# Kernel tuning notes

Hardware: AMD Instinct MI355X
Metric: run time of the kernel (lower is better)

## Reference

```python
import jax, jax.numpy as jnp
import numpy as np

EPS = 1e-5
P = 3  # p_size
BW = 1.0  # bandwidth


def _instance_norm(x):
    # calc_mean_std: per (B,C) mean/std over spatial dims, unbiased var (torch default)
    b, c, h, w = x.shape
    flat = x.reshape(b, c, h * w)
    mean = flat.mean(-1)[:, :, None, None]
    std = jnp.sqrt(flat.var(-1, ddof=1) + EPS)[:, :, None, None]
    return (x - mean) / std


def _conv1x1(x, w, bias):
    # x: (B,C,H,W), w: (O,C), bias: (O,)
    return jnp.einsum('oc,bchw->bohw', w, x) + bias[None, :, None, None]


def _patches_scaled(x, scale):
    # ReflectionPad2d(1) + Unfold(3) -> (B, HW, C*9), torch layout (c slow, k fast),
    # with ContextAtten scale applied over the 9 kernel positions.
    b, c, h, w = x.shape
    pad = jnp.pad(x, ((0, 0), (0, 0), (1, 1), (1, 1)), mode='reflect')
    # (B,C,H,W,9)
    p9 = jnp.stack([pad[:, :, di:di + h, dj:dj + w]
                    for di in range(P) for dj in range(P)], axis=-1)
    p9 = p9 * scale  # broadcast over last (kernel) axis
    # -> (B,H,W,C,9) -> (B, HW, C*9)
    return p9.transpose(0, 2, 3, 1, 4).reshape(b, h * w, c * P * P)


def setup_inputs() -> dict:
    key = jax.random.key(0)
    ks = jax.random.split(key, 12)
    B, C, H, W = 2, 512, 64, 64
    IC = 256
    f32 = jnp.float32
    inp = {
        'content': jax.random.normal(ks[0], (B, C, H, W), f32),
        'style': jax.random.normal(ks[1], (B, C, H, W), f32),
        'fusion_style': jax.random.normal(ks[2], (B, C, H, W), f32),
        'theta_w': jax.random.normal(ks[3], (IC, C), f32) * np.sqrt(2.0 / C),
        'theta_b': jnp.zeros((IC,), f32),
        'phi_w': jax.random.normal(ks[4], (IC, C), f32) * np.sqrt(2.0 / C),
        'phi_b': jnp.zeros((IC,), f32),
        'g_w': jax.random.normal(ks[5], (IC, C), f32) * np.sqrt(2.0 / C),
        'g_b': jnp.zeros((IC,), f32),
        'W_w': jax.random.normal(ks[6], (C, IC), f32) * np.sqrt(2.0 / IC),
        'W_b': jnp.zeros((C,), f32),
        'scale': jnp.ones((P * P,), f32),
    }
    return inp


def reference(content, style, fusion_style, theta_w, theta_b, phi_w, phi_b,
              g_w, g_b, W_w, W_b, scale):
    B, C, H, W = content.shape
    IC = theta_w.shape[0]
    HW = H * W

    # g on fusion_style -> (B, HW, IC)
    g_s = _conv1x1(fusion_style, g_w, g_b).reshape(B, IC, HW).transpose(0, 2, 1)

    # instance-normalize content/style (normal=True path)
    xn = _instance_norm(content)
    sn = _instance_norm(style)

    theta_x = _conv1x1(xn, theta_w, theta_b)
    phi_s = _conv1x1(sn, phi_w, phi_b)

    theta_p = _patches_scaled(theta_x, scale)  # (B, HW, IC*9)
    phi_p = _patches_scaled(phi_s, scale)      # (B, HW, IC*9)

    f = jnp.einsum('blk,bmk->blm', theta_p, phi_p) * BW  # (B, HW, HW)
    f_div_C = jax.nn.softmax(f, axis=-1)

    y = jnp.einsum('blm,bmo->blo', f_div_C, g_s)  # (B, HW, IC)
    y = y.transpose(0, 2, 1).reshape(B, IC, H, W)
    W_y = _conv1x1(y, W_w, W_b)  # (B, C, H, W)
    # isTraining=True path: conf_map = 0
    return W_y
```

## Files before the change

### kernel.cpp

```cpp
#include <hip/hip_runtime.h>
#include <stdint.h>

typedef __attribute__((ext_vector_type(8))) __bf16 bf16x8;
typedef __attribute__((ext_vector_type(4))) float f32x4;
typedef __attribute__((ext_vector_type(4))) unsigned int uint4v;

__device__ __forceinline__ float bf2f(unsigned short u){
  unsigned int x = ((unsigned int)u) << 16;
  return __builtin_bit_cast(float, x);
}
__device__ __forceinline__ unsigned short f2bf(float f){
  unsigned int x = __builtin_bit_cast(unsigned int, f);
  x += 0x7FFFu + ((x >> 16) & 1u);
  return (unsigned short)(x >> 16);
}

#define OUT_F32 0
#define OUT_BF16 1
#define OUT_SPLIT3 2
#define OUT_FLAG 3
#define OUT_PART 4
#define OUT_PARTH 5
#define BIAS_NONE 0
#define BIAS_ROW 1
#define BIAS_COL 2

template<int OM, int BM>
__global__ __launch_bounds__(256)
void gemm_bt(const unsigned short* __restrict__ A, int lda,
             const unsigned short* __restrict__ Bt, int ldb,
             int kchunk, void* __restrict__ Out, int ldo,
             const float* __restrict__ bias,
             int dupOff, int loOff,
             const unsigned int* __restrict__ flagPtr, size_t outOff,
             size_t zStride)
{
  __shared__ uint4v AsmBuf[1024];
  __shared__ uint4v BsmBuf[1024];
  char* Asm = (char*)AsmBuf;
  char* Bsm = (char*)BsmBuf;

  const unsigned int fl = (OM == OUT_FLAG) ? flagPtr[0] : 0u;

  const int tid  = threadIdx.x;
  const int lane = tid & 63;
  const int wave = tid >> 6;
  const int wy = wave >> 1, wx = wave & 1;
  const int lm = lane & 15, quad = lane >> 4;
  const int tileM = blockIdx.y * 128;
  const int tileN = blockIdx.x * 128;
  const int z = blockIdx.z;

  A  += (size_t)z * kchunk;
  Bt += (size_t)z * kchunk;

  const int sr0 = tid >> 2, sc0 = tid & 3;
  const int sr1 = sr0 + 64;
  const size_t gA0 = (size_t)(tileM + sr0)*lda + ((sc0 ^ ((sr0 >> 1) & 3)) << 3);
  const size_t gA1 = (size_t)(tileM + sr1)*lda + ((sc0 ^ ((sr1 >> 1) & 3)) << 3);
  const size_t gB0 = (size_t)(tileN + sr0)*ldb + ((sc0 ^ ((sr0 >> 1) & 3)) << 3);
  const size_t gB1 = (size_t)(tileN + sr1)*ldb + ((sc0 ^ ((sr1 >> 1) & 3)) << 3);
  const int lOff0 = sr0*64 + sc0*16;
  const int lOff1 = sr1*64 + sc0*16;

  int aOff[4], bOff[4];
#pragma unroll
  for (int t = 0; t < 4; ++t){
    int ra = wy*64 + t*16 + lm;
    aOff[t] = ra*64 + ((quad ^ ((ra >> 1) & 3)) << 4);
    int rb = wx*64 + t*16 + lm;
    bOff[t] = rb*64 + ((quad ^ ((rb >> 1) & 3)) << 4);
  }

  f32x4 acc[4][4] = {};

  const int ksteps = kchunk >> 5;
  uint4v a0v = *(const uint4v*)(A + gA0);
  uint4v a1v = *(const uint4v*)(A + gA1);
  uint4v b0v = *(const uint4v*)(Bt + gB0);
  uint4v b1v = *(const uint4v*)(Bt + gB1);

  for (int kt = 0; kt < ksteps; ++kt){
    char* As = Asm + (kt & 1)*8192;
    char* Bs = Bsm + (kt & 1)*8192;
    *(uint4v*)(As + lOff0) = a0v;
    *(uint4v*)(As + lOff1) = a1v;
    *(uint4v*)(Bs + lOff0) = b0v;
    *(uint4v*)(Bs + lOff1) = b1v;
    __syncthreads();
    if (kt + 1 < ksteps){
      const unsigned short* Ak = A + (kt + 1)*32;
      const unsigned short* Bk = Bt + (kt + 1)*32;
      a0v = *(const uint4v*)(Ak + gA0);
      a1v = *(const uint4v*)(Ak + gA1);
      b0v = *(const uint4v*)(Bk + gB0);
      b1v = *(const uint4v*)(Bk + gB1);
    }
    bf16x8 af[4], bfr[4];
#pragma unroll
    for (int t = 0; t < 4; ++t){
      af[t]  = __builtin_bit_cast(bf16x8, *(const uint4v*)(As + aOff[t]));
      bfr[t] = __builtin_bit_cast(bf16x8, *(const uint4v*)(Bs + bOff[t]));
    }
#pragma unroll
    for (int tm = 0; tm < 4; ++tm)
#pragma unroll
      for (int tn = 0; tn < 4; ++tn)
        acc[tm][tn] = __builtin_amdgcn_mfma_f32_16x16x32_bf16(af[tm], bfr[tn], acc[tm][tn], 0, 0, 0);
  }

#pragma unroll
  for (int tm = 0; tm < 4; ++tm){
    const int rowb = tileM + wy*64 + tm*16 + quad*4;
#pragma unroll
    for (int tn = 0; tn < 4; ++tn){
      const int col = tileN + wx*64 + tn*16 + lm;
      float bcv = 0.f;
      if (BM == BIAS_COL) bcv = bias[col];
#pragma unroll
      for (int r = 0; r < 4; ++r){
        float v = acc[tm][tn][r];
        const int row = rowb + r;
        if (BM == BIAS_ROW) v += bias[row];
        if (BM == BIAS_COL) v += bcv;
        const size_t idx = (size_t)row*ldo + col;
        if (OM == OUT_F32){
          ((float*)Out)[idx] = v;
        } else if (OM == OUT_BF16){
          ((unsigned short*)Out)[idx] = f2bf(v);
        } else if (OM == OUT_SPLIT3){
          unsigned short hi = f2bf(v);
          unsigned short lo = f2bf(v - bf2f(hi));
          unsigned short* O = (unsigned short*)Out;
          O[idx] = hi; O[idx + dupOff] = hi; O[idx + loOff] = lo;
        } else if (OM == OUT_PART){
          ((float*)Out)[(size_t)z*zStride + idx] = v;
        } else if (OM == OUT_PARTH){
          ((unsigned short*)Out)[(size_t)z*zStride + idx] = f2bf(v);
        } else {
          if (fl) ((float*)Out)[outOff + idx] = v;
          else    ((unsigned short*)Out)[outOff + idx] = f2bf(v);
        }
      }
    }
  }
}

__global__ __launch_bounds__(256)
void gemm_big(const unsigned short* __restrict__ A, int lda,
              const unsigned short* __restrict__ Bt, int ldb,
              int K, float* __restrict__ Out, int ldo)
{
  __shared__ uint4v AsmBuf[2048];
  __shared__ uint4v BsmBuf[1024];
  char* Asm = (char*)AsmBuf;
  char* Bsm = (char*)BsmBuf;

  const int tid  = threadIdx.x;
  const int lane = tid & 63;
  const int wave = tid >> 6;
  const int wy = wave >> 1, wx = wave & 1;
  const int lm = lane & 15, quad = lane >> 4;
  const int tileM = blockIdx.y * 256;
  const int tileN = blockIdx.x * 128;

  const int sr = tid >> 2, sc = tid & 3;
  size_t gA[4]; int lA[4];
  size_t gB[2]; int lB[2];
#pragma unroll
  for (int i = 0; i < 4; ++i){
    const int r = sr + 64*i;
    gA[i] = (size_t)(tileM + r)*lda + ((sc ^ ((r >> 1) & 3)) << 3);
    lA[i] = r*64 + sc*16;
  }
#pragma unroll
  for (int i = 0; i < 2; ++i){
    const int r = sr + 64*i;
    gB[i] = (size_t)(tileN + r)*ldb + ((sc ^ ((r >> 1) & 3)) << 3);
    lB[i] = r*64 + sc*16;
  }

  int aOff[8], bOff[4];
#pragma unroll
  for (int t = 0; t < 8; ++t){
    const int ra = wy*128 + t*16 + lm;
    aOff[t] = ra*64 + ((quad ^ ((ra >> 1) & 3)) << 4);
  }
#pragma unroll
  for (int t = 0; t < 4; ++t){
    const int rb = wx*64 + t*16 + lm;
    bOff[t] = rb*64 + ((quad ^ ((rb >> 1) & 3)) << 4);
  }

  f32x4 acc[8][4] = {};

  const int ksteps = K >> 5;
  uint4v av[4], bv[2];
#pragma unroll
  for (int i = 0; i < 4; ++i) av[i] = *(const uint4v*)(A + gA[i]);
#pragma unroll
  for (int i = 0; i < 2; ++i) bv[i] = *(const uint4v*)(Bt + gB[i]);

  for (int kt = 0; kt < ksteps; ++kt){
    char* As = Asm + (kt & 1)*16384;
    char* Bs = Bsm + (kt & 1)*8192;
#pragma unroll
    for (int i = 0; i < 4; ++i) *(uint4v*)(As + lA[i]) = av[i];
#pragma unroll
    for (int i = 0; i < 2; ++i) *(uint4v*)(Bs + lB[i]) = bv[i];
    __syncthreads();
    if (kt + 1 < ksteps){
      const unsigned short* Ak = A + (kt + 1)*32;
      const unsigned short* Bk = Bt + (kt + 1)*32;
#pragma unroll
      for (int i = 0; i < 4; ++i) av[i] = *(const uint4v*)(Ak + gA[i]);
#pragma unroll
      for (int i = 0; i < 2; ++i) bv[i] = *(const uint4v*)(Bk + gB[i]);
    }
    bf16x8 af[8], bfr[4];
#pragma unroll
    for (int t = 0; t < 8; ++t)
      af[t] = __builtin_bit_cast(bf16x8, *(const uint4v*)(As + aOff[t]));
#pragma unroll
    for (int t = 0; t < 4; ++t)
      bfr[t] = __builtin_bit_cast(bf16x8, *(const uint4v*)(Bs + bOff[t]));
#pragma unroll
    for (int tm = 0; tm < 8; ++tm)
#pragma unroll
      for (int tn = 0; tn < 4; ++tn)
        acc[tm][tn] = __builtin_amdgcn_mfma_f32_16x16x32_bf16(af[tm], bfr[tn], acc[tm][tn], 0, 0, 0);
  }

#pragma unroll
  for (int tm = 0; tm < 8; ++tm){
    const int rowb = tileM + wy*128 + tm*16 + quad*4;
#pragma unroll
    for (int tn = 0; tn < 4; ++tn){
      const int col = tileN + wx*64 + tn*16 + lm;
#pragma unroll
      for (int r = 0; r < 4; ++r)
        Out[(size_t)(rowb + r)*ldo + col] = acc[tm][tn][r];
    }
  }
}

template<int S, int OM, int BM, int CSH, bool HALFP>
__global__ __launch_bounds__(256)
void reduce_part(const void* __restrict__ part, size_t zStride,
                 const float* __restrict__ bias,
                 void* __restrict__ Out, int ldo,
                 int dupOff, int loOff,
                 const unsigned int* __restrict__ flagPtr, size_t outOff)
{
  const size_t i = (size_t)blockIdx.x*256 + threadIdx.x;
  const int row = (int)(i >> CSH);
  const int col = (int)(i & ((1u << CSH) - 1u));
  float v = 0.f;
#pragma unroll
  for (int s = 0; s < S; ++s){
    if (HALFP) v += bf2f(((const unsigned short*)part)[(size_t)s*zStride + i]);
    else       v += ((const float*)part)[(size_t)s*zStride + i];
  }
  if (BM == BIAS_ROW) v += bias[row];
  if (BM == BIAS_COL) v += bias[col];
  const size_t o = (size_t)row*ldo + col;
  if (OM == OUT_SPLIT3){
    unsigned short hi = f2bf(v);
    unsigned short lo = f2bf(v - bf2f(hi));
    unsigned short* O = (unsigned short*)Out;
    O[o] = hi; O[o + dupOff] = hi; O[o + loOff] = lo;
  } else if (OM == OUT_BF16){
    ((unsigned short*)Out)[o] = f2bf(v);
  } else {
    if (flagPtr[0]) ((float*)Out)[outOff + o] = v;
    else            ((unsigned short*)Out)[outOff + o] = f2bf(v);
  }
}

__global__ __launch_bounds__(256)
void detect_prep(const void* __restrict__ content,
                 const void* tb, const void* pb, const void* gb, const void* wb,
                 const void* sc,
                 unsigned int* __restrict__ flag, float* __restrict__ scale_c,
                 float* tb_c, float* pb_c, float* gb_c, float* wb_c)
{
  __shared__ int cnt;
  __shared__ unsigned int flg;
  const int tid = threadIdx.x;
  if (tid == 0) cnt = 0;
  __syncthreads();
  unsigned int w = ((const unsigned int*)content)[tid];
  int e = (w >> 23) & 0xFF;
  if (e >= 0x70 && e <= 0x8F) atomicAdd(&cnt, 1);
  __syncthreads();
  if (tid == 0){ flg = (cnt >= 128) ? 1u : 0u; flag[0] = flg; }
  __syncthreads();
  const unsigned int f = flg;
  auto rd = [&](const void* p, int i)->float{
    return f ? ((const float*)p)[i] : bf2f(((const unsigned short*)p)[i]);
  };
  if (tid < 9) scale_c[tid] = rd(sc, tid);
  tb_c[tid] = rd(tb, tid);
  pb_c[tid] = rd(pb, tid);
  gb_c[tid] = rd(gb, tid);
  wb_c[tid] = rd(wb, tid);
  wb_c[tid + 256] = rd(wb, tid + 256);
}

__global__ __launch_bounds__(256)
void conv_weights(const void* tw, const void* pw, const void* gw, const void* www,
                  const unsigned int* __restrict__ flagPtr,
                  unsigned short* __restrict__ wdup,
                  unsigned short* __restrict__ gwc,
                  unsigned short* __restrict__ wwc)
{
  const unsigned int fl = flagPtr[0];
  const int sec = blockIdx.y;
  const int idx = blockIdx.x*256 + threadIdx.x;
  auto rd = [&](const void* p, int i)->float{
    return fl ? ((const float*)p)[i] : bf2f(((const unsigned short*)p)[i]);
  };
  if (sec < 2){
    const void* w = sec ? pw : tw;
    const int o = idx >> 9, c = idx & 511;
    float v = rd(w, o*512 + c);
    unsigned short hi = f2bf(v);
    unsigned short lo = f2bf(v - bf2f(hi));
    unsigned short* base = wdup + (size_t)sec*256*1536 + o*1536;
    base[c] = hi; base[512 + c] = lo; base[1024 + c] = hi;
  } else if (sec == 2){
    const int o = idx >> 9, c = idx & 511;
    gwc[o*512 + c] = f2bf(rd(gw, o*512 + c));
  } else {
    const int o = idx >> 8, c = idx & 255;
    wwc[o*256 + c] = f2bf(rd(www, o*256 + c));
  }
}

__global__ __launch_bounds__(256)
void stats_kernel(const void* __restrict__ X, const unsigned int* __restrict__ flagPtr,
                  float* __restrict__ stats)
{
  const unsigned int fl = flagPtr[0];
  const int bc = blockIdx.x;
  const int tid = threadIdx.x;
  float s = 0.f, q = 0.f;
  if (fl){
    const f32x4* row = (const f32x4*)((const float*)X + (size_t)bc*4096);
#pragma unroll
    for (int i = 0; i < 4; ++i){
      f32x4 v = row[tid + i*256];
#pragma unroll
      for (int j = 0; j < 4; ++j){ s += v[j]; q += v[j]*v[j]; }
    }
  } else {
    const uint4v* row = (const uint4v*)((const unsigned short*)X + (size_t)bc*4096);
#pragma unroll
    for (int i = 0; i < 2; ++i){
      uint4v u = row[tid + i*256];
#pragma unroll
      for (int j = 0; j < 4; ++j){
        float a = bf2f((unsigned short)(u[j] & 0xffffu));
        float b = bf2f((unsigned short)(u[j] >> 16));
        s += a + b; q += a*a + b*b;
      }
    }
  }
#pragma unroll
  for (int off = 32; off > 0; off >>= 1){
    s += __shfl_down(s, off);
    q += __shfl_down(q, off);
  }
  __shared__ float rs[4], rq[4];
  if ((tid & 63) == 0){ rs[tid >> 6] = s; rq[tid >> 6] = q; }
  __syncthreads();
  if (tid == 0){
    s = rs[0] + rs[1] + rs[2] + rs[3];
    q = rq[0] + rq[1] + rq[2] + rq[3];
    float mean = s * (1.0f/4096.0f);
    float var  = (q - 4096.0f*mean*mean) * (1.0f/4095.0f);
    stats[bc*2 + 0] = mean;
    stats[bc*2 + 1] = 1.0f / sqrtf(var + 1e-5f);
  }
}

template<bool SPLIT>
__global__ __launch_bounds__(256)
void norm_transpose(const void* __restrict__ X, const float* __restrict__ stats,
                    unsigned short* __restrict__ Out,
                    const unsigned int* __restrict__ flagPtr)
{
  __shared__ float tile[64][65];
  const unsigned int fl = flagPtr[0];
  const int b  = blockIdx.z;
  const int l0 = blockIdx.x * 64;
  const int c0 = blockIdx.y * 64;
  const int tid = threadIdx.x;
  const int tx = tid & 63, ty = tid >> 6;

#pragma unroll
  for (int p = 0; p < 16; ++p){
    const int cc = ty + p*4;
    const size_t src = ((size_t)b*512 + c0 + cc)*4096 + l0 + tx;
    tile[cc][tx] = fl ? ((const float*)X)[src]
                      : bf2f(((const unsigned short*)X)[src]);
  }
  __syncthreads();
  float mean = 0.f, inv = 1.f;
  if (SPLIT){
    mean = stats[(b*512 + c0 + tx)*2 + 0];
    inv  = stats[(b*512 + c0 + tx)*2 + 1];
  }
#pragma unroll
  for (int p = 0; p < 16; ++p){
    const int lj = ty + p*4;
    const size_t rowOut = (size_t)b*4096 + l0 + lj;
    if (SPLIT){
      const float v = (tile[tx][lj] - mean) * inv;
      const size_t o = rowOut*1536 + c0 + tx;
      const unsigned short hi = f2bf(v);
      Out[o] = hi;
      Out[o + 512] = hi;
      Out[o + 1024] = f2bf(v - bf2f(hi));
    } else {
      const size_t o = rowOut*512 + c0 + tx;
      Out[o] = f2bf(tile[tx][lj]);
    }
  }
}

__global__ __launch_bounds__(256)
void softmax_rows(const float* __restrict__ G, const float* __restrict__ scale_c,
                  unsigned short* __restrict__ P)
{
  const int l = blockIdx.x;
  const int yy = l >> 6, xx = l & 63;
  const int tid = threadIdx.x;

  float s2[9];
  const float* rowp[9];
#pragma unroll
  for (int di = 0; di < 3; ++di){
    int ry = yy + di - 1; ry = ry < 0 ? 1 : (ry > 63 ? 62 : ry);
#pragma unroll
    for (int dj = 0; dj < 3; ++dj){
      int rx = xx + dj - 1; rx = rx < 0 ? 1 : (rx > 63 ? 62 : rx);
      const int k = di*3 + dj;
      const float s = scale_c[k];
      s2[k] = s*s;
      rowp[k] = G + (size_t)(ry*64 + rx)*4096;
    }
  }

  float fv[16];
  float mx = -3.0e38f;
#pragma unroll
  for (int i = 0; i < 16; ++i){
    const int m = tid + i*256;
    const int my = m >> 6, mxo = m & 63;
    int cy[3], cx[3];
#pragma unroll
    for (int d = 0; d < 3; ++d){
      int t0 = my + d - 1;  cy[d] = (t0 < 0 ? 1 : (t0 > 63 ? 62 : t0))*64;
      int t1 = mxo + d - 1; cx[d] = (t1 < 0 ? 1 : (t1 > 63 ? 62 : t1));
    }
    float v = 0.f;
#pragma unroll
    for (int di = 0; di < 3; ++di)
#pragma unroll
      for (int dj = 0; dj < 3; ++dj)
        v = fmaf(s2[di*3+dj], rowp[di*3+dj][cy[di] + cx[dj]], v);
    fv[i] = v;
    mx = fmaxf(mx, v);
  }

  __shared__ float redA[4], redB[4];
#pragma unroll
  for (int off = 32; off > 0; off >>= 1) mx = fmaxf(mx, __shfl_down(mx, off));
  if ((tid & 63) == 0) redA[tid >> 6] = mx;
  __syncthreads();
  mx = fmaxf(fmaxf(redA[0], redA[1]), fmaxf(redA[2], redA[3]));

  float sum = 0.f;
#pragma unroll
  for (int i = 0; i < 16; ++i){ fv[i] = __expf(fv[i] - mx); sum += fv[i]; }
#pragma unroll
  for (int off = 32; off > 0; off >>= 1) sum += __shfl_down(sum, off);
  if ((tid & 63) == 0) redB[tid >> 6] = sum;
  __syncthreads();
  sum = redB[0] + redB[1] + redB[2] + redB[3];
  const float inv = 1.0f / sum;

  unsigned short* Prow = P + (size_t)l*4096;
#pragma unroll
  for (int i = 0; i < 16; ++i) Prow[tid + i*256] = f2bf(fv[i]*inv);
}

extern "C" void kernel_launch(void* const* d_in, const int* in_sizes, int n_in,
                              void* d_out, int out_size, void* d_ws, size_t ws_size,
                              hipStream_t stream)
{
  const void* content = d_in[0];
  const void* style   = d_in[1];
  const void* fusion  = d_in[2];
  const void* theta_w = d_in[3];
  const void* theta_b = d_in[4];
  const void* phi_w   = d_in[5];
  const void* phi_b   = d_in[6];
  const void* g_w     = d_in[7];
  const void* g_b     = d_in[8];
  const void* W_w     = d_in[9];
  const void* W_b     = d_in[10];
  const void* scale   = d_in[11];

  char* ws = (char*)d_ws;
  size_t off = 0;
  auto take = [&](size_t bytes)->char*{
    char* p = ws + off; off += (bytes + 255) & ~(size_t)255; return p;
  };

  unsigned int* flag  = (unsigned int*)take(256);
  float* scale_c      = (float*)take(256);
  float* tb_c         = (float*)take(1024);
  float* pb_c         = (float*)take(1024);
  float* gb_c         = (float*)take(1024);
  float* wb_c         = (float*)take(2048);
  float* statsC       = (float*)take(1024ull*2*4);
  float* statsS       = (float*)take(1024ull*2*4);
  unsigned short* wdup = (unsigned short*)take(2ull*256*1536*2);
  unsigned short* gwc  = (unsigned short*)take(256ull*512*2);
  unsigned short* wwc  = (unsigned short*)take(512ull*256*2);
  unsigned short* th   = (unsigned short*)take(8192ull*768*2);
  unsigned short* ph   = (unsigned short*)take(8192ull*768*2);
  unsigned short* gs   = (unsigned short*)take(256ull*8192*2);
  unsigned short* yb   = (unsigned short*)take(2ull*4096*256*2);
  float* G             = (float*)take(4096ull*4096*4);
  char* unionC         = take(2ull*4096*1536*2*2 + 2ull*4096*512*2);
  unsigned short* xn   = (unsigned short*)unionC;
  unsigned short* sn   = (unsigned short*)(unionC + 8192ull*1536*2);
  unsigned short* fst  = (unsigned short*)(unionC + 2ull*8192*1536*2);
  unsigned short* P    = (unsigned short*)unionC;
  float* partF          = G;
  unsigned short* partH = (unsigned short*)G;
  const size_t zTP = 8192ull*256;
  const size_t zG  = 256ull*8192;
  const size_t zY  = 4096ull*256;
  const size_t zW  = 512ull*4096;

  detect_prep<<<1, 256, 0, stream>>>(content, theta_b, phi_b, g_b, W_b, scale,
                                     flag, scale_c, tb_c, pb_c, gb_c, wb_c);
  conv_weights<<<dim3(512,4), 256, 0, stream>>>(theta_w, phi_w, g_w, W_w, flag,
                                                wdup, gwc, wwc);
  stats_kernel<<<1024, 256, 0, stream>>>(content, flag, statsC);
  stats_kernel<<<1024, 256, 0, stream>>>(style,   flag, statsS);
  dim3 ntg(64, 8, 2);
  norm_transpose<true ><<<ntg, 256, 0, stream>>>(content, statsC, xn, flag);
  norm_transpose<true ><<<ntg, 256, 0, stream>>>(style,   statsS, sn, flag);
  norm_transpose<false><<<ntg, 256, 0, stream>>>(fusion,  nullptr, fst, flag);

  gemm_bt<OUT_PART, BIAS_NONE><<<dim3(2,64,4), 256, 0, stream>>>(
      xn, 1536, wdup, 1536, 384, partF, 256, nullptr, 0, 0, nullptr, 0, zTP);
  reduce_part<4, OUT_SPLIT3, BIAS_COL, 8, false><<<8192, 256, 0, stream>>>(
      partF, zTP, tb_c, th, 768, 256, 512, nullptr, 0);
  gemm_bt<OUT_PART, BIAS_NONE><<<dim3(2,64,4), 256, 0, stream>>>(
      sn, 1536, wdup + 256*1536, 1536, 384, partF, 256, nullptr, 0, 0, nullptr, 0, zTP);
  reduce_part<4, OUT_SPLIT3, BIAS_COL, 8, false><<<8192, 256, 0, stream>>>(
      partF, zTP, pb_c, ph, 768, 512, 256, nullptr, 0);
  gemm_bt<OUT_PARTH, BIAS_NONE><<<dim3(64,2,4), 256, 0, stream>>>(
      gwc, 512, fst, 512, 128, partH, 8192, nullptr, 0, 0, nullptr, 0, zG);
  reduce_part<4, OUT_BF16, BIAS_ROW, 13, true><<<8192, 256, 0, stream>>>(
      partH, zG, gb_c, gs, 8192, 0, 0, nullptr, 0);

  for (int b = 0; b < 2; ++b){
    const unsigned short* thb = th + (size_t)b*4096*768;
    const unsigned short* phb = ph + (size_t)b*4096*768;
    gemm_big<<<dim3(32,16), 256, 0, stream>>>(thb, 768, phb, 768, 768, G, 4096);
    softmax_rows<<<4096, 256, 0, stream>>>(G, scale_c, P);
    gemm_bt<OUT_PARTH, BIAS_NONE><<<dim3(2,32,8), 256, 0, stream>>>(
        P, 4096, gs + (size_t)b*4096, 8192, 512, partH, 256, nullptr, 0, 0, nullptr, 0, zY);
    reduce_part<8, OUT_BF16, BIAS_NONE, 8, true><<<4096, 256, 0, stream>>>(
        partH, zY, nullptr, yb + (size_t)b*4096*256, 256, 0, 0, nullptr, 0);
    gemm_bt<OUT_PART, BIAS_NONE><<<dim3(32,4,2), 256, 0, stream>>>(
        wwc, 256, yb + (size_t)b*4096*256, 256, 128, partF, 4096, nullptr, 0, 0, nullptr, 0, zW);
    reduce_part<2, OUT_FLAG, BIAS_ROW, 12, false><<<8192, 256, 0, stream>>>(
        partF, zW, wb_c, d_out, 4096, 0, 0, flag, (size_t)b*512*4096);
  }
}
```

Before: 418.4 us.

## Batch per-batch and per-input launches into single grid-z kernels

Merges the two batch iterations and the paired content/style/fusion launches into single launches by indexing the batch or input through blockIdx.z. The stats, normalize, projection GEMMs, the big similarity GEMM, softmax, the aggregation GEMM and the output GEMM each run once with a doubled grid, and a second 64 MB score buffer is allocated so both batches' scores coexist. Reductions get specialized kernels. This is meant to cut launch count and fill the GPU better on the smaller GEMMs, at the cost of more memory footprint.

```diff
diff --git a/kernel.cpp b/kernel.cpp
--- a/kernel.cpp
+++ b/kernel.cpp
@@ -15,32 +15,21 @@
   return (unsigned short)(x >> 16);
 }
 
-#define OUT_F32 0
-#define OUT_BF16 1
-#define OUT_SPLIT3 2
-#define OUT_FLAG 3
 #define OUT_PART 4
 #define OUT_PARTH 5
-#define BIAS_NONE 0
-#define BIAS_ROW 1
-#define BIAS_COL 2
-
-template<int OM, int BM>
+
+template<int OM>
 __global__ __launch_bounds__(256)
 void gemm_bt(const unsigned short* __restrict__ A, int lda,
              const unsigned short* __restrict__ Bt, int ldb,
              int kchunk, void* __restrict__ Out, int ldo,
-             const float* __restrict__ bias,
-             int dupOff, int loOff,
-             const unsigned int* __restrict__ flagPtr, size_t outOff,
-             size_t zStride)
+             size_t zStride, size_t aBatch, size_t bBatch,
+             int sMask, int sShift)
 {
   __shared__ uint4v AsmBuf[1024];
   __shared__ uint4v BsmBuf[1024];
   char* Asm = (char*)AsmBuf;
   char* Bsm = (char*)BsmBuf;
-
-  const unsigned int fl = (OM == OUT_FLAG) ? flagPtr[0] : 0u;
 
   const int tid  = threadIdx.x;
   const int lane = tid & 63;
@@ -50,9 +39,11 @@
   const int tileM = blockIdx.y * 128;
   const int tileN = blockIdx.x * 128;
   const int z = blockIdx.z;
-
-  A  += (size_t)z * kchunk;
-  Bt += (size_t)z * kchunk;
+  const int slice = z & sMask;
+  const int batch = z >> sShift;
+
+  A  += (size_t)slice*kchunk + (size_t)batch*aBatch;
+  Bt += (size_t)slice*kchunk + (size_t)batch*bBatch;
 
   const int sr0 = tid >> 2, sc0 = tid & 3;
   const int sr1 = sr0 + 64;
@@ -115,32 +106,12 @@
 #pragma unroll
     for (int tn = 0; tn < 4; ++tn){
       const int col = tileN + wx*64 + tn*16 + lm;
-      float bcv = 0.f;
-      if (BM == BIAS_COL) bcv = bias[col];
 #pragma unroll
       for (int r = 0; r < 4; ++r){
-        float v = acc[tm][tn][r];
-        const int row = rowb + r;
-        if (BM == BIAS_ROW) v += bias[row];
-        if (BM == BIAS_COL) v += bcv;
-        const size_t idx = (size_t)row*ldo + col;
-        if (OM == OUT_F32){
-          ((float*)Out)[idx] = v;
-        } else if (OM == OUT_BF16){
-          ((unsigned short*)Out)[idx] = f2bf(v);
-        } else if (OM == OUT_SPLIT3){
-          unsigned short hi = f2bf(v);
-          unsigned short lo = f2bf(v - bf2f(hi));
-          unsigned short* O = (unsigned short*)Out;
-          O[idx] = hi; O[idx + dupOff] = hi; O[idx + loOff] = lo;
-        } else if (OM == OUT_PART){
-          ((float*)Out)[(size_t)z*zStride + idx] = v;
-        } else if (OM == OUT_PARTH){
-          ((unsigned short*)Out)[(size_t)z*zStride + idx] = f2bf(v);
-        } else {
-          if (fl) ((float*)Out)[outOff + idx] = v;
-          else    ((unsigned short*)Out)[outOff + idx] = f2bf(v);
-        }
+        const float v = acc[tm][tn][r];
+        const size_t idx = (size_t)z*zStride + (size_t)(rowb + r)*ldo + col;
+        if (OM == OUT_PART) ((float*)Out)[idx] = v;
+        else                ((unsigned short*)Out)[idx] = f2bf(v);
       }
     }
   }
@@ -149,7 +120,8 @@
 __global__ __launch_bounds__(256)
 void gemm_big(const unsigned short* __restrict__ A, int lda,
               const unsigned short* __restrict__ Bt, int ldb,
-              int K, float* __restrict__ Out, int ldo)
+              int K, float* __restrict__ Out, int ldo,
+              size_t aBatch, size_t bBatch, size_t oBatch)
 {
   __shared__ uint4v AsmBuf[2048];
   __shared__ uint4v BsmBuf[1024];
@@ -163,6 +135,11 @@
   const int lm = lane & 15, quad = lane >> 4;
   const int tileM = blockIdx.y * 256;
   const int tileN = blockIdx.x * 128;
+  const int z = blockIdx.z;
+
+  A  += (size_t)z*aBatch;
+  Bt += (size_t)z*bBatch;
+  Out += (size_t)z*oBatch;
 
   const int sr = tid >> 2, sc = tid & 3;
   size_t gA[4]; int lA[4];
@@ -244,37 +221,66 @@
   }
 }
 
-template<int S, int OM, int BM, int CSH, bool HALFP>
-__global__ __launch_bounds__(256)
-void reduce_part(const void* __restrict__ part, size_t zStride,
-                 const float* __restrict__ bias,
-                 void* __restrict__ Out, int ldo,
-                 int dupOff, int loOff,
-                 const unsigned int* __restrict__ flagPtr, size_t outOff)
+__global__ __launch_bounds__(256)
+void reduce_tp(const float* __restrict__ part,
+               const float* __restrict__ tb, const float* __restrict__ pb,
+               unsigned short* __restrict__ th, unsigned short* __restrict__ ph)
 {
   const size_t i = (size_t)blockIdx.x*256 + threadIdx.x;
-  const int row = (int)(i >> CSH);
-  const int col = (int)(i & ((1u << CSH) - 1u));
+  const int which = (int)(i >> 21);
+  const size_t j = i & 0x1FFFFFu;
+  const int col = (int)(j & 255u);
   float v = 0.f;
 #pragma unroll
-  for (int s = 0; s < S; ++s){
-    if (HALFP) v += bf2f(((const unsigned short*)part)[(size_t)s*zStride + i]);
-    else       v += ((const float*)part)[(size_t)s*zStride + i];
-  }
-  if (BM == BIAS_ROW) v += bias[row];
-  if (BM == BIAS_COL) v += bias[col];
-  const size_t o = (size_t)row*ldo + col;
-  if (OM == OUT_SPLIT3){
-    unsigned short hi = f2bf(v);
-    unsigned short lo = f2bf(v - bf2f(hi));
-    unsigned short* O = (unsigned short*)Out;
-    O[o] = hi; O[o + dupOff] = hi; O[o + loOff] = lo;
-  } else if (OM == OUT_BF16){
-    ((unsigned short*)Out)[o] = f2bf(v);
-  } else {
-    if (flagPtr[0]) ((float*)Out)[outOff + o] = v;
-    else            ((unsigned short*)Out)[outOff + o] = f2bf(v);
-  }
+  for (int s = 0; s < 4; ++s)
+    v += part[(size_t)((which << 2) + s)*2097152 + j];
+  v += (which ? pb : tb)[col];
+  unsigned short hi = f2bf(v);
+  unsigned short lo = f2bf(v - bf2f(hi));
+  const size_t o = (j >> 8)*768 + col;
+  unsigned short* O = which ? ph : th;
+  const int dup = which ? 512 : 256;
+  const int loo = which ? 256 : 512;
+  O[o] = hi; O[o + dup] = hi; O[o + loo] = lo;
+}
+
+__global__ __launch_bounds__(256)
+void reduce_g(const unsigned short* __restrict__ part,
+              const float* __restrict__ gb, unsigned short* __restrict__ gs)
+{
+  const size_t i = (size_t)blockIdx.x*256 + threadIdx.x;
+  float v = 0.f;
+#pragma unroll
+  for (int s = 0; s < 4; ++s) v += bf2f(part[(size_t)s*2097152 + i]);
+  gs[i] = f2bf(v + gb[i >> 13]);
+}
+
+__global__ __launch_bounds__(256)
+void reduce_y(const unsigned short* __restrict__ part,
+              unsigned short* __restrict__ yb)
+{
+  const size_t i = (size_t)blockIdx.x*256 + threadIdx.x;
+  const int b = (int)(i >> 20);
+  const size_t j = i & 0xFFFFFu;
+  float v = 0.f;
+#pragma unroll
+  for (int s = 0; s < 8; ++s)
+    v += bf2f(part[(size_t)((b << 3) + s)*1048576 + j]);
+  yb[i] = f2bf(v);
+}
+
+__global__ __launch_bounds__(256)
+void reduce_w(const float* __restrict__ part, const float* __restrict__ wb,
+              void* __restrict__ Out, const unsigned int* __restrict__ flagPtr)
+{
+  const size_t i = (size_t)blockIdx.x*256 + threadIdx.x;
+  const int b = (int)(i >> 21);
+  const size_t j = i & 0x1FFFFFu;
+  float v = part[(size_t)(b << 1)*2097152 + j]
+          + part[(size_t)((b << 1) | 1)*2097152 + j]
+          + wb[(i >> 12) & 511u];
+  if (flagPtr[0]) ((float*)Out)[i] = v;
+  else            ((unsigned short*)Out)[i] = f2bf(v);
 }
 
 __global__ __launch_bounds__(256)
@@ -338,10 +344,13 @@
 }
 
 __global__ __launch_bounds__(256)
-void stats_kernel(const void* __restrict__ X, const unsigned int* __restrict__ flagPtr,
-                  float* __restrict__ stats)
+void stats_all(const void* __restrict__ content, const void* __restrict__ style,
+               const unsigned int* __restrict__ flagPtr,
+               float* __restrict__ statsC, float* __restrict__ statsS)
 {
   const unsigned int fl = flagPtr[0];
+  const void* X = blockIdx.z ? style : content;
+  float* stats = blockIdx.z ? statsS : statsC;
   const int bc = blockIdx.x;
   const int tid = threadIdx.x;
   float s = 0.f, q = 0.f;
@@ -384,20 +393,25 @@
   }
 }
 
-template<bool SPLIT>
-__global__ __launch_bounds__(256)
-void norm_transpose(const void* __restrict__ X, const float* __restrict__ stats,
-                    unsigned short* __restrict__ Out,
-                    const unsigned int* __restrict__ flagPtr)
+__global__ __launch_bounds__(256)
+void norm_all(const void* __restrict__ content, const void* __restrict__ style,
+              const void* __restrict__ fusion,
+              const float* __restrict__ statsC, const float* __restrict__ statsS,
+              unsigned short* __restrict__ xn, unsigned short* __restrict__ sn,
+              unsigned short* __restrict__ fst,
+              const unsigned int* __restrict__ flagPtr)
 {
   __shared__ float tile[64][65];
   const unsigned int fl = flagPtr[0];
-  const int b  = blockIdx.z;
+  const int z = blockIdx.z;
+  const int which = z >> 1;
+  const int b  = z & 1;
   const int l0 = blockIdx.x * 64;
   const int c0 = blockIdx.y * 64;
   const int tid = threadIdx.x;
   const int tx = tid & 63, ty = tid >> 6;
 
+  const void* X = which == 0 ? content : (which == 1 ? style : fusion);
 #pragma unroll
   for (int p = 0; p < 16; ++p){
     const int cc = ty + p*4;
@@ -406,34 +420,39 @@
                       : bf2f(((const unsigned short*)X)[src]);
   }
   __syncthreads();
-  float mean = 0.f, inv = 1.f;
-  if (SPLIT){
-    mean = stats[(b*512 + c0 + tx)*2 + 0];
-    inv  = stats[(b*512 + c0 + tx)*2 + 1];
-  }
-#pragma unroll
-  for (int p = 0; p < 16; ++p){
-    const int lj = ty + p*4;
-    const size_t rowOut = (size_t)b*4096 + l0 + lj;
-    if (SPLIT){
+  if (which < 2){
+    const float* stats = which ? statsS : statsC;
+    const float mean = stats[(b*512 + c0 + tx)*2 + 0];
+    const float inv  = stats[(b*512 + c0 + tx)*2 + 1];
+    unsigned short* Out = which ? sn : xn;
+#pragma unroll
+    for (int p = 0; p < 16; ++p){
+      const int lj = ty + p*4;
       const float v = (tile[tx][lj] - mean) * inv;
-      const size_t o = rowOut*1536 + c0 + tx;
+      const size_t o = ((size_t)b*4096 + l0 + lj)*1536 + c0 + tx;
       const unsigned short hi = f2bf(v);
       Out[o] = hi;
       Out[o + 512] = hi;
       Out[o + 1024] = f2bf(v - bf2f(hi));
-    } else {
-      const size_t o = rowOut*512 + c0 + tx;
-      Out[o] = f2bf(tile[tx][lj]);
-    }
-  }
-}
-
-__global__ __launch_bounds__(256)
-void softmax_rows(const float* __restrict__ G, const float* __restrict__ scale_c,
-                  unsigned short* __restrict__ P)
-{
-  const int l = blockIdx.x;
+    }
+  } else {
+#pragma unroll
+    for (int p = 0; p < 16; ++p){
+      const int lj = ty + p*4;
+      const size_t o = ((size_t)b*4096 + l0 + lj)*512 + c0 + tx;
+      fst[o] = f2bf(tile[tx][lj]);
+    }
+  }
+}
+
+__global__ __launch_bounds__(256)
+void softmax_rows(const float* __restrict__ Gbase, const float* __restrict__ scale_c,
+                  unsigned short* __restrict__ Pbase)
+{
+  const int bb = blockIdx.x >> 12;
+  const int l  = blockIdx.x & 4095;
+  const float* G = Gbase + (size_t)bb*16777216;
+  unsigned short* P = Pbase + (size_t)bb*16777216;
   const int yy = l >> 6, xx = l & 63;
   const int tid = threadIdx.x;
 
@@ -534,55 +553,49 @@
   unsigned short* ph   = (unsigned short*)take(8192ull*768*2);
   unsigned short* gs   = (unsigned short*)take(256ull*8192*2);
   unsigned short* yb   = (unsigned short*)take(2ull*4096*256*2);
-  float* G             = (float*)take(4096ull*4096*4);
-  char* unionC         = take(2ull*4096*1536*2*2 + 2ull*4096*512*2);
+  float* G0            = (float*)take(4096ull*4096*4);
+  float* G1            = (float*)take(4096ull*4096*4);
+  char* unionC         = take(64ull*1024*1024);
   unsigned short* xn   = (unsigned short*)unionC;
   unsigned short* sn   = (unsigned short*)(unionC + 8192ull*1536*2);
   unsigned short* fst  = (unsigned short*)(unionC + 2ull*8192*1536*2);
   unsigned short* P    = (unsigned short*)unionC;
-  float* partF          = G;
-  unsigned short* partH = (unsigned short*)G;
-  const size_t zTP = 8192ull*256;
-  const size_t zG  = 256ull*8192;
-  const size_t zY  = 4096ull*256;
-  const size_t zW  = 512ull*4096;
+
+  float* partTP          = G0;
+  unsigned short* partG  = (unsigned short*)G1;
+  unsigned short* partY  = (unsigned short*)G0;
+  float* partW           = G1;
 
   detect_prep<<<1, 256, 0, stream>>>(content, theta_b, phi_b, g_b, W_b, scale,
                                      flag, scale_c, tb_c, pb_c, gb_c, wb_c);
   conv_weights<<<dim3(512,4), 256, 0, stream>>>(theta_w, phi_w, g_w, W_w, flag,
                                                 wdup, gwc, wwc);
-  stats_kernel<<<1024, 256, 0, stream>>>(content, flag, statsC);
-  stats_kernel<<<1024, 256, 0, stream>>>(style,   flag, statsS);
-  dim3 ntg(64, 8, 2);
-  norm_transpose<true ><<<ntg, 256, 0, stream>>>(content, statsC, xn, flag);
-  norm_transpose<true ><<<ntg, 256, 0, stream>>>(style,   statsS, sn, flag);
-  norm_transpose<false><<<ntg, 256, 0, stream>>>(fusion,  nullptr, fst, flag);
-
-  gemm_bt<OUT_PART, BIAS_NONE><<<dim3(2,64,4), 256, 0, stream>>>(
-      xn, 1536, wdup, 1536, 384, partF, 256, nullptr, 0, 0, nullptr, 0, zTP);
-  reduce_part<4, OUT_SPLIT3, BIAS_COL, 8, false><<<8192, 256, 0, stream>>>(
-      partF, zTP, tb_c, th, 768, 256, 512, nullptr, 0);
-  gemm_bt<OUT_PART, BIAS_NONE><<<dim3(2,64,4), 256, 0, stream>>>(
-      sn, 1536, wdup + 256*1536, 1536, 384, partF, 256, nullptr, 0, 0, nullptr, 0, zTP);
-  reduce_part<4, OUT_SPLIT3, BIAS_COL, 8, false><<<8192, 256, 0, stream>>>(
-      partF, zTP, pb_c, ph, 768, 512, 256, nullptr, 0);
-  gemm_bt<OUT_PARTH, BIAS_NONE><<<dim3(64,2,4), 256, 0, stream>>>(
-      gwc, 512, fst, 512, 128, partH, 8192, nullptr, 0, 0, nullptr, 0, zG);
-  reduce_part<4, OUT_BF16, BIAS_ROW, 13, true><<<8192, 256, 0, stream>>>(
-      partH, zG, gb_c, gs, 8192, 0, 0, nullptr, 0);
-
-  for (int b = 0; b < 2; ++b){
-    const unsigned short* thb = th + (size_t)b*4096*768;
-    const unsigned short* phb = ph + (size_t)b*4096*768;
-    gemm_big<<<dim3(32,16), 256, 0, stream>>>(thb, 768, phb, 768, 768, G, 4096);
-    softmax_rows<<<4096, 256, 0, stream>>>(G, scale_c, P);
-    gemm_bt<OUT_PARTH, BIAS_NONE><<<dim3(2,32,8), 256, 0, stream>>>(
-        P, 4096, gs + (size_t)b*4096, 8192, 512, partH, 256, nullptr, 0, 0, nullptr, 0, zY);
-    reduce_part<8, OUT_BF16, BIAS_NONE, 8, true><<<4096, 256, 0, stream>>>(
-        partH, zY, nullptr, yb + (size_t)b*4096*256, 256, 0, 0, nullptr, 0);
-    gemm_bt<OUT_PART, BIAS_NONE><<<dim3(32,4,2), 256, 0, stream>>>(
-        wwc, 256, yb + (size_t)b*4096*256, 256, 128, partF, 4096, nullptr, 0, 0, nullptr, 0, zW);
-    reduce_part<2, OUT_FLAG, BIAS_ROW, 12, false><<<8192, 256, 0, stream>>>(
-        partF, zW, wb_c, d_out, 4096, 0, 0, flag, (size_t)b*512*4096);
-  }
-}
+  stats_all<<<dim3(1024,1,2), 256, 0, stream>>>(content, style, flag, statsC, statsS);
+  norm_all<<<dim3(64,8,6), 256, 0, stream>>>(content, style, fusion,
+                                             statsC, statsS, xn, sn, fst, flag);
+
+  gemm_bt<OUT_PART><<<dim3(2,64,8), 256, 0, stream>>>(
+      xn, 1536, wdup, 1536, 384, partTP, 256, 8192ull*256,
+      8192ull*1536, 256ull*1536, 3, 2);
+  reduce_tp<<<16384, 256, 0, stream>>>(partTP, tb_c, pb_c, th, ph);
+
+  gemm_bt<OUT_PARTH><<<dim3(64,2,4), 256, 0, stream>>>(
+      gwc, 512, fst, 512, 128, partG, 8192, 256ull*8192, 0, 0, 3, 2);
+  reduce_g<<<8192, 256, 0, stream>>>(partG, gb_c, gs);
+
+  gemm_big<<<dim3(32,16,2), 256, 0, stream>>>(
+      th, 768, ph, 768, 768, G0, 4096,
+      4096ull*768, 4096ull*768, (size_t)(G1 - G0));
+
+  softmax_rows<<<8192, 256, 0, stream>>>(G0, scale_c, P);
+
+  gemm_bt<OUT_PARTH><<<dim3(2,32,16), 256, 0, stream>>>(
+      P, 4096, gs, 8192, 512, partY, 256, 4096ull*256,
+      16777216ull, 4096ull, 7, 3);
+  reduce_y<<<8192, 256, 0, stream>>>(partY, yb);
+
+  gemm_bt<OUT_PART><<<dim3(32,4,4), 256, 0, stream>>>(
+      wwc, 256, yb, 256, 128, partW, 4096, 512ull*4096,
+      0, 4096ull*256, 1, 1);
+  reduce_w<<<16384, 256, 0, stream>>>(partW, wb_c, d_out, flag);
+}
```

New measurement: 394.5 us. 5.7% less time.
